# Kernel tuning notes

Measured on AMD Instinct MI355X. Metric: run time of the kernel, lower is better.

The kernel has to match this reference:

```python
import jax, jax.numpy as jnp
import numpy as np


def setup_inputs() -> dict:
    key = jax.random.key(0)
    k1, k2 = jax.random.split(key)
    B, C, H, W = 16, 256, 64, 64
    K, D = 1024, 256
    z = jax.random.normal(k1, (B, C, H, W), dtype=jnp.float32)
    embedding = jax.random.normal(k2, (K, D), dtype=jnp.float32)
    return {"z": z, "embedding": embedding}


def reference(z, embedding):
    # _preprocess: shift channel dim (axis 1) to last, flatten -> [N, D]
    B, C, H, W = z.shape
    encoded_permuted = jnp.transpose(z, (0, 2, 3, 1))  # [B, H, W, C]
    permuted_shape = encoded_permuted.shape
    encoded_flat = encoded_permuted.reshape(-1, C)  # [N, D]

    x_sq = jnp.sum(encoded_flat * encoded_flat, axis=1, keepdims=True)  # [N, 1]
    e_sq = jnp.sum(embedding * embedding, axis=1)  # [K]
    cross = encoded_flat @ embedding.T  # [N, K]
    distances = x_sq - 2.0 * cross + e_sq[None, :]
    codebook_indices = jnp.argmin(distances, axis=1)  # [N]
    quantized_lookup = embedding[codebook_indices]  # [N, D]

    # straight-through estimator
    quantized_flat = encoded_flat + jax.lax.stop_gradient(quantized_lookup - encoded_flat)

    # _postprocess: reshape and shift last dim back to axis 1
    quantized = jnp.transpose(quantized_flat.reshape(permuted_shape), (0, 3, 1, 2))
    return (encoded_flat, quantized_flat, codebook_indices, quantized)
```

## Files before the change

### kernel.cpp

```cpp
#include <hip/hip_runtime.h>
#include <hip/hip_bf16.h>

typedef _Float16 h8 __attribute__((ext_vector_type(8)));
typedef float f4 __attribute__((ext_vector_type(4)));

#define N_TOK 65536
#define DIM 256
#define KCODES 1024
#define HWSZ 4096

__device__ __forceinline__ void gll16(const void* g, void* l) {
    __builtin_amdgcn_global_load_lds((const __attribute__((address_space(1))) void*)g,
                                     (__attribute__((address_space(3))) void*)l, 16, 0, 0);
}


__global__ void k_prep_frag(const float* __restrict__ emb, _Float16* __restrict__ BhF,
                            _Float16* __restrict__ BlF) {
    int gi = blockIdx.x * 256 + threadIdx.x;
    int kb = gi >> 9;
    int s = (gi >> 6) & 7;
    int dq = (gi >> 4) & 3;
    int r = gi & 15;
    int code = kb * 16 + r;
    int d0 = s * 32 + dq * 8;
    const float* src = emb + (size_t)code * DIM + d0;
    float4 x0 = *(const float4*)(src);
    float4 x1 = *(const float4*)(src + 4);
    float xs[8] = {x0.x, x0.y, x0.z, x0.w, x1.x, x1.y, x1.z, x1.w};
    h8 hi, lo;
#pragma unroll
    for (int j = 0; j < 8; ++j) {
        _Float16 h = (_Float16)xs[j];
        hi[j] = h;
        lo[j] = (_Float16)(xs[j] - (float)h);
    }
    *(h8*)(BhF + (size_t)gi * 8) = hi;
    *(h8*)(BlF + (size_t)gi * 8) = lo;
}

__global__ void k_esq(const float* __restrict__ emb, float* __restrict__ e_sq) {
    int t = threadIdx.x;
    int code = blockIdx.x * 4 + (t >> 6);
    int l = t & 63;
    float4 v = *(const float4*)(emb + (size_t)code * DIM + l * 4);
    float s = v.x * v.x + v.y * v.y + v.z * v.z + v.w * v.w;
#pragma unroll
    for (int off = 32; off >= 1; off >>= 1) s += __shfl_xor(s, off);
    if (l == 0) e_sq[code] = s;
}

__global__ void k_transpose(const float* __restrict__ z, float* __restrict__ enc,
                            _Float16* __restrict__ AhF, _Float16* __restrict__ AlF) {
    __shared__ float T[64][65];
    int blk = blockIdx.x;
    int b = blk >> 8;
    int rem = blk & 255;
    int c0 = (rem >> 6) * 64;
    int hw0 = (rem & 63) * 64;
    int t = threadIdx.x;
    const float* zp = z + (size_t)b * DIM * HWSZ;
    {
        int hw4 = (t & 15) * 4, cl = t >> 4;
#pragma unroll
        for (int i = 0; i < 4; ++i) {
            int c = cl + i * 16;
            float4 v = *(const float4*)(zp + (size_t)(c0 + c) * HWSZ + hw0 + hw4);
            T[c][hw4 + 0] = v.x; T[c][hw4 + 1] = v.y;
            T[c][hw4 + 2] = v.z; T[c][hw4 + 3] = v.w;
        }
    }
    __syncthreads();
    {
        int c4 = (t & 15) * 4, hwl = t >> 4;
#pragma unroll
        for (int i = 0; i < 4; ++i) {
            int hw = hwl + i * 16;
            float4 v;
            v.x = T[c4 + 0][hw]; v.y = T[c4 + 1][hw];
            v.z = T[c4 + 2][hw]; v.w = T[c4 + 3][hw];
            *(float4*)(enc + (size_t)(b * HWSZ + hw0 + hw) * DIM + c0 + c4) = v;
        }
    }
    {
        int base_nb = b * 256 + (hw0 >> 4);
#pragma unroll
        for (int i = 0; i < 2; ++i) {
            int gidx = i * 256 + t;
            int nbi = gidx >> 7;
            int si = (gidx >> 6) & 1;
            int dq = (gidx >> 4) & 3;
            int r = gidx & 15;
            int hwl = nbi * 16 + r;
            int cl = si * 32 + dq * 8;
            h8 hi, lo;
#pragma unroll
            for (int j = 0; j < 8; ++j) {
                float x = T[cl + j][hwl];
                _Float16 h = (_Float16)x;
                hi[j] = h;
                lo[j] = (_Float16)(x - (float)h);
            }
            size_t G = (((size_t)(base_nb + nbi) * 8) + (c0 >> 5) + si) * 64 + dq * 16 + r;
            *(h8*)(AhF + G * 8) = hi;
            *(h8*)(AlF + G * 8) = lo;
        }
    }
}

#define WAITV(n) asm volatile("s_waitcnt vmcnt(" #n ")" ::: "memory")
#define BARRIER __builtin_amdgcn_s_barrier()
#define PRIO1 __builtin_amdgcn_s_setprio(1)
#define PRIO0 __builtin_amdgcn_s_setprio(0)

extern __shared__ char SB[];

__global__ __launch_bounds__(1024)
void k_gemm_argmin(const _Float16* __restrict__ AhF, const _Float16* __restrict__ AlF,
                   const _Float16* __restrict__ BhF, const _Float16* __restrict__ BlF,
                   const float* __restrict__ e_sq,
                   float* __restrict__ pV1, int* __restrict__ pI1) {
    int gid = blockIdx.x;
    int grp = gid >> 7;
    int colTile = (gid >> 5) & 3;
    int rowTile = grp * 32 + (gid & 31);
    int r0 = rowTile * 256, c0 = colTile * 256;
    int t = threadIdx.x;
    int w = t >> 6, l = t & 63;
    int wm = w >> 2, wn = w & 3;
    int l16 = l & 15, lhi = l >> 4;

    const char* gAh = (const char*)AhF + (((size_t)(rowTile * 16 + w)) << 13) + (l << 4);
    const char* gAl = (const char*)AlF + (((size_t)(rowTile * 16 + w)) << 13) + (l << 4);
    const char* gBh = (const char*)BhF + (((size_t)(colTile * 16 + w)) << 13) + (l << 4);
    const char* gBl = (const char*)BlF + (((size_t)(colTile * 16 + w)) << 13) + (l << 4);

#define ISSUE_P(p) do { \
    const int s_ = (p) >> 1; \
    char* bp_ = SB + ((p) & 3) * 32768; \
    const char* a_ = ((p) & 1) ? gAl : gAh; \
    const char* b_ = ((p) & 1) ? gBl : gBh; \
    gll16(a_ + (s_ << 10), bp_ + (w << 10)); \
    gll16(b_ + (s_ << 10), bp_ + 16384 + (w << 10)); \
} while (0)

#define MFMA16(A_, B_) { _Pragma("unroll") for (int mf = 0; mf < 4; ++mf) \
    _Pragma("unroll") for (int nf = 0; nf < 4; ++nf) \
        acc[mf][nf] = __builtin_amdgcn_mfma_f32_16x16x32_f16(A_[mf], B_[nf], acc[mf][nf], 0, 0, 0); }

#define PHASE(q, W, DO_ISSUE) { \
    WAITV(W); \
    BARRIER; \
    if (DO_ISSUE) ISSUE_P((q) + 3); \
    const char* bp_ = SB + ((q) & 3) * 32768; \
    if (((q) & 1) == 0) { \
        _Pragma("unroll") for (int mf = 0; mf < 4; ++mf) \
            ah[mf] = *(const h8*)(bp_ + ((wm * 4 + mf) << 10) + (l << 4)); \
        _Pragma("unroll") for (int nf = 0; nf < 4; ++nf) \
            bh[nf] = *(const h8*)(bp_ + 16384 + ((wn * 4 + nf) << 10) + (l << 4)); \
        PRIO1; MFMA16(ah, bh); PRIO0; \
    } else { \
        h8 xl[4]; \
        _Pragma("unroll") for (int nf = 0; nf < 4; ++nf) \
            xl[nf] = *(const h8*)(bp_ + 16384 + ((wn * 4 + nf) << 10) + (l << 4)); \
        PRIO1; MFMA16(ah, xl); PRIO0; \
        _Pragma("unroll") for (int mf = 0; mf < 4; ++mf) \
            xl[mf] = *(const h8*)(bp_ + ((wm * 4 + mf) << 10) + (l << 4)); \
        PRIO1; MFMA16(xl, bh); PRIO0; \
    } }

    f4 acc[4][4];
#pragma unroll
    for (int i = 0; i < 4; ++i)
#pragma unroll
        for (int j = 0; j < 4; ++j) acc[i][j] = (f4)0.0f;

    h8 ah[4], bh[4];

    ISSUE_P(0); ISSUE_P(1); ISSUE_P(2);

    PHASE(0, 4, 1)   PHASE(1, 4, 1)   PHASE(2, 4, 1)   PHASE(3, 4, 1)
    PHASE(4, 4, 1)   PHASE(5, 4, 1)   PHASE(6, 4, 1)   PHASE(7, 4, 1)
    PHASE(8, 4, 1)   PHASE(9, 4, 1)   PHASE(10, 4, 1)  PHASE(11, 4, 1)
    PHASE(12, 4, 1)  PHASE(13, 4, 0)  PHASE(14, 2, 0)  PHASE(15, 0, 0)

    float* smV = (float*)SB;
    int* smI = (int*)(SB + 4096);

    float esq[4];
#pragma unroll
    for (int nf = 0; nf < 4; ++nf) esq[nf] = e_sq[c0 + wn * 64 + nf * 16 + l16];

#pragma unroll
    for (int mf = 0; mf < 4; ++mf) {
#pragma unroll
        for (int rg = 0; rg < 4; ++rg) {
            float bestV = 3.4e38f;
            int bestI = 0;
#pragma unroll
            for (int nf = 0; nf < 4; ++nf) {
                float v = esq[nf] - 2.0f * acc[mf][nf][rg];
                int ci = c0 + wn * 64 + nf * 16 + l16;
                if (v < bestV || (v == bestV && ci < bestI)) { bestV = v; bestI = ci; }
            }
#pragma unroll
            for (int off = 1; off < 16; off <<= 1) {
                float vv = __shfl_xor(bestV, off);
                int ii = __shfl_xor(bestI, off);
                if (vv < bestV || (vv == bestV && ii < bestI)) { bestV = vv; bestI = ii; }
            }
            if (l16 == 0) {
                int rloc = wm * 64 + mf * 16 + lhi * 4 + rg;
                smV[wn * 256 + rloc] = bestV;
                smI[wn * 256 + rloc] = bestI;
            }
        }
    }
    __syncthreads();
    if (t < 256) {
        float bestV = smV[t];
        int bestI = smI[t];
#pragma unroll
        for (int wn2 = 1; wn2 < 4; ++wn2) {
            float v = smV[wn2 * 256 + t];
            int i2 = smI[wn2 * 256 + t];
            if (v < bestV || (v == bestV && i2 < bestI)) { bestV = v; bestI = i2; }
        }
        pV1[colTile * N_TOK + r0 + t] = bestV;
        pI1[colTile * N_TOK + r0 + t] = bestI;
    }
}

__global__ void k_final_out1(const float* __restrict__ pV1, const int* __restrict__ pI1,
                             const float* __restrict__ emb,
                             float* __restrict__ out2, int* __restrict__ idxI,
                             float* __restrict__ out1) {
    __shared__ int sidx[256];
    int t = threadIdx.x;
    int n0 = blockIdx.x * 256;
    int n = n0 + t;
    float v1 = pV1[n];
    int i1 = pI1[n];
#pragma unroll
    for (int ct = 1; ct < 4; ++ct) {
        float a1 = pV1[ct * N_TOK + n];
        int ai = pI1[ct * N_TOK + n];
        if (a1 < v1 || (a1 == v1 && ai < i1)) { v1 = a1; i1 = ai; }
    }
    out2[n] = (float)i1;
    idxI[n] = i1;
    sidx[t] = i1;
    __syncthreads();
    int rr = t >> 2, q = t & 3;
#pragma unroll
    for (int i = 0; i < 4; ++i) {
        int r = i * 64 + rr;
        int idx = sidx[r];
        const float* src = emb + (size_t)idx * DIM + q * 64;
        float* dst = out1 + (size_t)(n0 + r) * DIM + q * 64;
#pragma unroll
        for (int j = 0; j < 16; ++j)
            *(float4*)(dst + j * 4) = *(const float4*)(src + j * 4);
    }
}

__global__ void k_out3(const float* __restrict__ emb, const int* __restrict__ idxI,
                       float* __restrict__ out3) {
    __shared__ float E[32][257];
    int blk = blockIdx.x;
    int b = blk >> 7, hwt = blk & 127;
    int hw0 = hwt * 32;
    int n0 = b * HWSZ + hw0;
    int t = threadIdx.x;
    {
        int r = t >> 3, oct = t & 7;
        int idx = idxI[n0 + r];
        const float* src = emb + (size_t)idx * DIM + oct * 32;
#pragma unroll
        for (int i = 0; i < 8; ++i) {
            float4 v = *(const float4*)(src + i * 4);
            E[r][oct * 32 + i * 4 + 0] = v.x;
            E[r][oct * 32 + i * 4 + 1] = v.y;
            E[r][oct * 32 + i * 4 + 2] = v.z;
            E[r][oct * 32 + i * 4 + 3] = v.w;
        }
    }
    __syncthreads();
    {
        int w = t >> 6, l = t & 63;
        int ch = l >> 5, hw = l & 31;
        float* dst = out3 + (size_t)b * DIM * HWSZ + hw0 + hw;
#pragma unroll
        for (int it = 0; it < 32; ++it) {
            int c = w * 64 + it * 2 + ch;
            dst[(size_t)c * HWSZ] = E[hw][c];
        }
    }
}

extern "C" void kernel_launch(void* const* d_in, const int* in_sizes, int n_in,
                              void* d_out, int out_size, void* d_ws, size_t ws_size,
                              hipStream_t stream) {
    const float* z = (const float*)d_in[0];
    const float* emb = (const float*)d_in[1];
    float* out = (float*)d_out;
    float* out0 = out;
    float* out1 = out + 16777216;
    float* out2 = out + 33554432;
    float* out3 = out + 33619968;

    _Float16* AhF = (_Float16*)out1;
    _Float16* AlF = (_Float16*)(out1 + 8388608);

    char* ws = (char*)d_ws;
    _Float16* BhF = (_Float16*)(ws);
    _Float16* BlF = (_Float16*)(ws + 524288);
    float* e_sq = (float*)(ws + 1048576);
    float* pV1 = (float*)(ws + 1052672);
    int* pI1 = (int*)(ws + 2101248);
    int* idxI = (int*)(ws + 3149824);

    hipFuncSetAttribute((const void*)k_gemm_argmin,
                        hipFuncAttributeMaxDynamicSharedMemorySize, 131072);

    k_prep_frag<<<128, 256, 0, stream>>>(emb, BhF, BlF);
    k_esq<<<256, 256, 0, stream>>>(emb, e_sq);
    k_transpose<<<4096, 256, 0, stream>>>(z, out0, AhF, AlF);
    k_gemm_argmin<<<1024, 1024, 131072, stream>>>(AhF, AlF, BhF, BlF, e_sq, pV1, pI1);
    k_final_out1<<<256, 256, 0, stream>>>(pV1, pI1, emb, out2, idxI, out1);
    k_out3<<<2048, 256, 0, stream>>>(emb, idxI, out3);
}
```

Before: 205.6 us.

## Restructure GEMM pipeline to double-buffered stages and fuse output kernels

The GEMM main loop now loads hi and lo fragments for a whole K-stage together into one of two 64KB buffers, replacing the previous 4-slot pipeline that ran three phases ahead. It waits for all outstanding loads before each stage, which shortens prefetch depth and may expose more memory latency. Separately, the out1 gather and the transposed out3 write are fused into a single kernel launched on 256 blocks, with each block looping over 8 sub-tiles. This removes the idxI round trip and one launch, but gives the out3 work far fewer blocks than the previous 2048.

Result: no change. 205.4 us (median of 2 runs) (-0.1%).

```diff
diff --git a/kernel.cpp b/kernel.cpp
--- a/kernel.cpp
+++ b/kernel.cpp
@@ -18,13 +18,9 @@
 __global__ void k_prep_frag(const float* __restrict__ emb, _Float16* __restrict__ BhF,
                             _Float16* __restrict__ BlF) {
     int gi = blockIdx.x * 256 + threadIdx.x;
-    int kb = gi >> 9;
-    int s = (gi >> 6) & 7;
-    int dq = (gi >> 4) & 3;
-    int r = gi & 15;
+    int kb = gi >> 9, s = (gi >> 6) & 7, dq = (gi >> 4) & 3, r = gi & 15;
     int code = kb * 16 + r;
-    int d0 = s * 32 + dq * 8;
-    const float* src = emb + (size_t)code * DIM + d0;
+    const float* src = emb + (size_t)code * DIM + s * 32 + dq * 8;
     float4 x0 = *(const float4*)(src);
     float4 x1 = *(const float4*)(src + 4);
     float xs[8] = {x0.x, x0.y, x0.z, x0.w, x1.x, x1.y, x1.z, x1.w};
@@ -87,10 +83,7 @@
 #pragma unroll
         for (int i = 0; i < 2; ++i) {
             int gidx = i * 256 + t;
-            int nbi = gidx >> 7;
-            int si = (gidx >> 6) & 1;
-            int dq = (gidx >> 4) & 3;
-            int r = gidx & 15;
+            int nbi = gidx >> 7, si = (gidx >> 6) & 1, dq = (gidx >> 4) & 3, r = gidx & 15;
             int hwl = nbi * 16 + r;
             int cl = si * 32 + dq * 8;
             h8 hi, lo;
@@ -135,39 +128,35 @@
     const char* gBh = (const char*)BhF + (((size_t)(colTile * 16 + w)) << 13) + (l << 4);
     const char* gBl = (const char*)BlF + (((size_t)(colTile * 16 + w)) << 13) + (l << 4);
 
-#define ISSUE_P(p) do { \
-    const int s_ = (p) >> 1; \
-    char* bp_ = SB + ((p) & 3) * 32768; \
-    const char* a_ = ((p) & 1) ? gAl : gAh; \
-    const char* b_ = ((p) & 1) ? gBl : gBh; \
-    gll16(a_ + (s_ << 10), bp_ + (w << 10)); \
-    gll16(b_ + (s_ << 10), bp_ + 16384 + (w << 10)); \
+#define ISSUE_S(s) do { \
+    char* bp_ = SB + ((s) & 1) * 65536; \
+    gll16(gAh + ((s) << 10), bp_ + (w << 10)); \
+    gll16(gBh + ((s) << 10), bp_ + 16384 + (w << 10)); \
+    gll16(gAl + ((s) << 10), bp_ + 32768 + (w << 10)); \
+    gll16(gBl + ((s) << 10), bp_ + 49152 + (w << 10)); \
 } while (0)
 
 #define MFMA16(A_, B_) { _Pragma("unroll") for (int mf = 0; mf < 4; ++mf) \
     _Pragma("unroll") for (int nf = 0; nf < 4; ++nf) \
         acc[mf][nf] = __builtin_amdgcn_mfma_f32_16x16x32_f16(A_[mf], B_[nf], acc[mf][nf], 0, 0, 0); }
 
-#define PHASE(q, W, DO_ISSUE) { \
-    WAITV(W); \
+#define PHASE(q, DO_ISSUE) { \
+    WAITV(0); \
     BARRIER; \
-    if (DO_ISSUE) ISSUE_P((q) + 3); \
-    const char* bp_ = SB + ((q) & 3) * 32768; \
-    if (((q) & 1) == 0) { \
-        _Pragma("unroll") for (int mf = 0; mf < 4; ++mf) \
-            ah[mf] = *(const h8*)(bp_ + ((wm * 4 + mf) << 10) + (l << 4)); \
-        _Pragma("unroll") for (int nf = 0; nf < 4; ++nf) \
-            bh[nf] = *(const h8*)(bp_ + 16384 + ((wn * 4 + nf) << 10) + (l << 4)); \
-        PRIO1; MFMA16(ah, bh); PRIO0; \
-    } else { \
-        h8 xl[4]; \
-        _Pragma("unroll") for (int nf = 0; nf < 4; ++nf) \
-            xl[nf] = *(const h8*)(bp_ + 16384 + ((wn * 4 + nf) << 10) + (l << 4)); \
-        PRIO1; MFMA16(ah, xl); PRIO0; \
-        _Pragma("unroll") for (int mf = 0; mf < 4; ++mf) \
-            xl[mf] = *(const h8*)(bp_ + ((wm * 4 + mf) << 10) + (l << 4)); \
-        PRIO1; MFMA16(xl, bh); PRIO0; \
-    } }
+    if (DO_ISSUE) ISSUE_S((q) + 1); \
+    const char* bp_ = SB + ((q) & 1) * 65536; \
+    _Pragma("unroll") for (int mf = 0; mf < 4; ++mf) \
+        ah[mf] = *(const h8*)(bp_ + ((wm * 4 + mf) << 10) + (l << 4)); \
+    _Pragma("unroll") for (int nf = 0; nf < 4; ++nf) \
+        bh[nf] = *(const h8*)(bp_ + 16384 + ((wn * 4 + nf) << 10) + (l << 4)); \
+    PRIO1; MFMA16(ah, bh); PRIO0; \
+    { h8 xl[4]; \
+      _Pragma("unroll") for (int nf = 0; nf < 4; ++nf) \
+          xl[nf] = *(const h8*)(bp_ + 49152 + ((wn * 4 + nf) << 10) + (l << 4)); \
+      PRIO1; MFMA16(ah, xl); PRIO0; \
+      _Pragma("unroll") for (int mf = 0; mf < 4; ++mf) \
+          xl[mf] = *(const h8*)(bp_ + 32768 + ((wm * 4 + mf) << 10) + (l << 4)); \
+      PRIO1; MFMA16(xl, bh); PRIO0; } }
 
     f4 acc[4][4];
 #pragma unroll
@@ -177,12 +166,10 @@
 
     h8 ah[4], bh[4];
 
-    ISSUE_P(0); ISSUE_P(1); ISSUE_P(2);
-
-    PHASE(0, 4, 1)   PHASE(1, 4, 1)   PHASE(2, 4, 1)   PHASE(3, 4, 1)
-    PHASE(4, 4, 1)   PHASE(5, 4, 1)   PHASE(6, 4, 1)   PHASE(7, 4, 1)
-    PHASE(8, 4, 1)   PHASE(9, 4, 1)   PHASE(10, 4, 1)  PHASE(11, 4, 1)
-    PHASE(12, 4, 1)  PHASE(13, 4, 0)  PHASE(14, 2, 0)  PHASE(15, 0, 0)
+    ISSUE_S(0);
+
+    PHASE(0, 1)  PHASE(1, 1)  PHASE(2, 1)  PHASE(3, 1)
+    PHASE(4, 1)  PHASE(5, 1)  PHASE(6, 1)  PHASE(7, 0)
 
     float* smV = (float*)SB;
     int* smI = (int*)(SB + 4096);
@@ -231,11 +218,12 @@
     }
 }
 
-__global__ void k_final_out1(const float* __restrict__ pV1, const int* __restrict__ pI1,
-                             const float* __restrict__ emb,
-                             float* __restrict__ out2, int* __restrict__ idxI,
-                             float* __restrict__ out1) {
+__global__ void k_final_all(const float* __restrict__ pV1, const int* __restrict__ pI1,
+                            const float* __restrict__ emb,
+                            float* __restrict__ out2, float* __restrict__ out1,
+                            float* __restrict__ out3) {
     __shared__ int sidx[256];
+    __shared__ float E[32][257];
     int t = threadIdx.x;
     int n0 = blockIdx.x * 256;
     int n = n0 + t;
@@ -248,52 +236,48 @@
         if (a1 < v1 || (a1 == v1 && ai < i1)) { v1 = a1; i1 = ai; }
     }
     out2[n] = (float)i1;
-    idxI[n] = i1;
     sidx[t] = i1;
     __syncthreads();
-    int rr = t >> 2, q = t & 3;
-#pragma unroll
-    for (int i = 0; i < 4; ++i) {
-        int r = i * 64 + rr;
-        int idx = sidx[r];
-        const float* src = emb + (size_t)idx * DIM + q * 64;
-        float* dst = out1 + (size_t)(n0 + r) * DIM + q * 64;
-#pragma unroll
-        for (int j = 0; j < 16; ++j)
-            *(float4*)(dst + j * 4) = *(const float4*)(src + j * 4);
-    }
-}
-
-__global__ void k_out3(const float* __restrict__ emb, const int* __restrict__ idxI,
-                       float* __restrict__ out3) {
-    __shared__ float E[32][257];
-    int blk = blockIdx.x;
-    int b = blk >> 7, hwt = blk & 127;
-    int hw0 = hwt * 32;
-    int n0 = b * HWSZ + hw0;
-    int t = threadIdx.x;
     {
-        int r = t >> 3, oct = t & 7;
-        int idx = idxI[n0 + r];
-        const float* src = emb + (size_t)idx * DIM + oct * 32;
-#pragma unroll
-        for (int i = 0; i < 8; ++i) {
-            float4 v = *(const float4*)(src + i * 4);
-            E[r][oct * 32 + i * 4 + 0] = v.x;
-            E[r][oct * 32 + i * 4 + 1] = v.y;
-            E[r][oct * 32 + i * 4 + 2] = v.z;
-            E[r][oct * 32 + i * 4 + 3] = v.w;
-        }
-    }
-    __syncthreads();
-    {
-        int w = t >> 6, l = t & 63;
-        int ch = l >> 5, hw = l & 31;
-        float* dst = out3 + (size_t)b * DIM * HWSZ + hw0 + hw;
-#pragma unroll
-        for (int it = 0; it < 32; ++it) {
-            int c = w * 64 + it * 2 + ch;
-            dst[(size_t)c * HWSZ] = E[hw][c];
+        int rr = t >> 2, q = t & 3;
+#pragma unroll
+        for (int i = 0; i < 4; ++i) {
+            int r = i * 64 + rr;
+            int idx = sidx[r];
+            const float* src = emb + (size_t)idx * DIM + q * 64;
+            float* dst = out1 + (size_t)(n0 + r) * DIM + q * 64;
+#pragma unroll
+            for (int j = 0; j < 16; ++j)
+                *(float4*)(dst + j * 4) = *(const float4*)(src + j * 4);
+        }
+    }
+    int b = n0 >> 12;
+    int hw0b = n0 & 4095;
+    for (int sub = 0; sub < 8; ++sub) {
+        __syncthreads();
+        {
+            int r = t >> 3, oct = t & 7;
+            int idx = sidx[sub * 32 + r];
+            const float* src = emb + (size_t)idx * DIM + oct * 32;
+#pragma unroll
+            for (int i = 0; i < 8; ++i) {
+                float4 v = *(const float4*)(src + i * 4);
+                E[r][oct * 32 + i * 4 + 0] = v.x;
+                E[r][oct * 32 + i * 4 + 1] = v.y;
+                E[r][oct * 32 + i * 4 + 2] = v.z;
+                E[r][oct * 32 + i * 4 + 3] = v.w;
+            }
+        }
+        __syncthreads();
+        {
+            int w = t >> 6, l = t & 63;
+            int ch = l >> 5, hw = l & 31;
+            float* dst = out3 + (size_t)b * DIM * HWSZ + hw0b + sub * 32 + hw;
+#pragma unroll
+            for (int it = 0; it < 32; ++it) {
+                int c = w * 64 + it * 2 + ch;
+                dst[(size_t)c * HWSZ] = E[hw][c];
+            }
         }
     }
 }
@@ -318,7 +302,6 @@
     float* e_sq = (float*)(ws + 1048576);
     float* pV1 = (float*)(ws + 1052672);
     int* pI1 = (int*)(ws + 2101248);
-    int* idxI = (int*)(ws + 3149824);
 
     hipFuncSetAttribute((const void*)k_gemm_argmin,
                         hipFuncAttributeMaxDynamicSharedMemorySize, 131072);
@@ -327,6 +310,5 @@
     k_esq<<<256, 256, 0, stream>>>(emb, e_sq);
     k_transpose<<<4096, 256, 0, stream>>>(z, out0, AhF, AlF);
     k_gemm_argmin<<<1024, 1024, 131072, stream>>>(AhF, AlF, BhF, BlF, e_sq, pV1, pI1);
-    k_final_out1<<<256, 256, 0, stream>>>(pV1, pI1, emb, out2, idxI, out1);
-    k_out3<<<2048, 256, 0, stream>>>(emb, idxI, out3);
-}
+    k_final_all<<<256, 256, 0, stream>>>(pV1, pI1, emb, out2, out1, out3);
+}
```
